# Kernel tuning notes

Hardware: AMD Instinct MI355X
Metric: run time of the kernel (lower is better)

## Reference

```python
import jax, jax.numpy as jnp
import numpy as np
from jax import lax

SIGMA = 2.0      # init arg
HIGH = 0.2       # init arg: high_threshold
LOW = 0.1        # skimage canny default low_threshold for float images
MAX_ITERS = 256  # cap for hysteresis propagation


def _conv2(img, kern):
    # img (N,1,H,W), kern (kh,kw); reflect-padded 'same' convolution
    kh, kw = kern.shape
    p = jnp.pad(img, ((0, 0), (0, 0), (kh // 2, kh // 2), (kw // 2, kw // 2)), mode='reflect')
    k = kern[None, None].astype(img.dtype)
    return lax.conv_general_dilated(p, k, (1, 1), 'VALID')


def _canny(x):
    # x (N,1,H,W) in [0,1] -> binary edge maps (N,H,W) float32
    r = int(4.0 * SIGMA + 0.5)
    g1 = np.exp(-0.5 * (np.arange(-r, r + 1) / SIGMA) ** 2)
    g1 = (g1 / g1.sum()).astype(np.float32)
    # separable gaussian blur
    sm = _conv2(_conv2(x, jnp.asarray(g1[:, None])), jnp.asarray(g1[None, :]))
    # sobel gradients
    sob = jnp.asarray([[-1., 0., 1.], [-2., 0., 2.], [-1., 0., 1.]], jnp.float32)
    gx = _conv2(sm, sob)[:, 0]
    gy = _conv2(sm, sob.T)[:, 0]          # (N,H,W)
    mag = jnp.hypot(gx, gy)
    ang = jnp.degrees(jnp.arctan2(gy, gx)) % 180.0
    N, H, W = mag.shape
    mp = jnp.pad(mag, ((0, 0), (1, 1), (1, 1)))
    sh = lambda dy, dx: mp[:, 1 + dy:1 + dy + H, 1 + dx:1 + dx + W]
    # quantize gradient direction into 4 bins for non-max suppression
    b0 = (ang < 22.5) | (ang >= 157.5)            # horizontal gradient -> E/W neighbors
    b1 = (ang >= 22.5) & (ang < 67.5)             # 45 deg
    b2 = (ang >= 67.5) & (ang < 112.5)            # vertical
    n1 = jnp.where(b0, sh(0, 1), jnp.where(b1, sh(-1, 1), jnp.where(b2, sh(-1, 0), sh(-1, -1))))
    n2 = jnp.where(b0, sh(0, -1), jnp.where(b1, sh(1, -1), jnp.where(b2, sh(1, 0), sh(1, 1))))
    keep = (mag >= n1) & (mag >= n2)
    strong = keep & (mag > HIGH)
    weak = keep & (mag > LOW)

    def dilate(s):
        f = lax.reduce_window(s.astype(jnp.float32), -jnp.inf, lax.max, (1, 3, 3), (1, 1, 1), 'SAME')
        return f > 0.0

    # hysteresis: propagate strong labels through weak pixels until fixpoint
    def cond(c):
        return c[1] & (c[2] < MAX_ITERS)

    def body(c):
        s, _, it = c
        ns = (dilate(s) & weak) | s
        return ns, jnp.any(ns != s), it + 1

    strong, _, _ = lax.while_loop(cond, body, (strong, jnp.array(True), jnp.array(0, jnp.int32)))
    return strong.astype(jnp.float32)


def setup_inputs() -> dict:
    key = jax.random.key(0)
    k1, k2, k3 = jax.random.split(key, 3)
    N, H, W = 16, 1024, 1024
    x = jax.random.uniform(k1, (N, 1, H, W), jnp.float32)
    y = jax.random.uniform(k2, (N, 1, H, W), jnp.float32)
    mask = jax.random.uniform(k3, (H, W), jnp.float32)
    return {"x": x, "y": y, "mask": mask}


def reference(x, y, mask):
    # original detaches x before canny -> edges carry no gradient
    edges = lax.stop_gradient(_canny(x))          # (N,H,W)
    # sum over batch of per-sample mean L1 (nn.L1Loss default reduction='mean')
    diff = jnp.abs(edges * mask - y[:, 0] * mask)
    return jnp.sum(jnp.mean(diff, axis=(1, 2)))
```

## Files before the change

### kernel.cpp

```cpp
#include <hip/hip_runtime.h>
#include <cmath>

#define IMG_W   1024
#define IMG_H   1024
#define NIMG    16
#define HW      (1024 * 1024)
#define NHW     (16 * 1024 * 1024)
#define WPR     16
#define WPI     (IMG_H * WPR)

struct GW { float w[9]; };

__device__ __forceinline__ int refl(int v) {
    return v < 0 ? -v : (v > 1023 ? 2046 - v : v);
}

__global__ void blur_v(const float* __restrict__ in, float* __restrict__ out, GW g) {
    int gid = blockIdx.x * 256 + threadIdx.x;
    int c4  = gid & 255;
    int rc  = (gid >> 8) & 127;
    const float* img = in  + (size_t)(gid >> 15) * HW;
    float*      outp = out + (size_t)(gid >> 15) * HW;
    int y0 = rc * 8;
    float4 acc[8];
#pragma unroll
    for (int j = 0; j < 8; ++j) acc[j] = make_float4(0.f, 0.f, 0.f, 0.f);
#pragma unroll
    for (int d = -8; d <= 15; ++d) {
        int rr = refl(y0 + d);
        float4 v = *(const float4*)(img + rr * IMG_W + c4 * 4);
#pragma unroll
        for (int j = 0; j < 8; ++j) {
            int k = d - j;
            if (k >= -8 && k <= 8) {
                float wt = g.w[k < 0 ? -k : k];
                acc[j].x += wt * v.x; acc[j].y += wt * v.y;
                acc[j].z += wt * v.z; acc[j].w += wt * v.w;
            }
        }
    }
#pragma unroll
    for (int j = 0; j < 8; ++j)
        *(float4*)(outp + (y0 + j) * IMG_W + c4 * 4) = acc[j];
}

__global__ void __launch_bounds__(256)
hgradnms(const float* __restrict__ vb, unsigned long long* __restrict__ strongw,
         unsigned long long* __restrict__ weakw, GW g) {
    __shared__ float smem[68 * 84 + 68 * 72];
    float* VB = smem;
    float* S  = smem + 68 * 84;
    float* M  = smem;
    unsigned char* Bn = (unsigned char*)(smem + 66 * 68);

    int tid = threadIdx.x;
    int b   = blockIdx.x;
    int img = b >> 8;
    int tr  = (b >> 4) & 15, tc = b & 15;
    int r0  = tr * 64, c0 = tc * 64;
    const float* vimg = vb + (size_t)img * HW;

    for (int i = tid; i < 68 * 84; i += 256) {
        int l = i / 84, m = i % 84;
        int gr = refl(r0 + l - 2);
        int gc = refl(c0 + m - 10);
        VB[i] = vimg[gr * IMG_W + gc];
    }
    __syncthreads();

    for (int i = tid; i < 68 * 17; i += 256) {
        int l = i / 17, grp = i % 17;
        const float4* p = (const float4*)(VB + l * 84 + 4 * grp);
        float w20[20];
        ((float4*)w20)[0] = p[0]; ((float4*)w20)[1] = p[1]; ((float4*)w20)[2] = p[2];
        ((float4*)w20)[3] = p[3]; ((float4*)w20)[4] = p[4];
        float o[4] = {0.f, 0.f, 0.f, 0.f};
#pragma unroll
        for (int t = 0; t < 17; ++t) {
            float wt = g.w[t < 8 ? 8 - t : t - 8];
#pragma unroll
            for (int j = 0; j < 4; ++j) o[j] += wt * w20[j + t];
        }
        *(float4*)(S + l * 72 + 4 * grp) = make_float4(o[0], o[1], o[2], o[3]);
    }
    __syncthreads();

    const float T1 = 0.41421356237309503f;
    const float T2 = 2.41421356237309510f;
    for (int i = tid; i < 66 * 17; i += 256) {
        int row = i / 17, grp = i % 17;
        float ra[8], rb[8], rcw[8];
        ((float4*)ra)[0]  = *(const float4*)(S + (row    ) * 72 + 4 * grp);
        ((float4*)ra)[1]  = *(const float4*)(S + (row    ) * 72 + 4 * grp + 4);
        ((float4*)rb)[0]  = *(const float4*)(S + (row + 1) * 72 + 4 * grp);
        ((float4*)rb)[1]  = *(const float4*)(S + (row + 1) * 72 + 4 * grp + 4);
        ((float4*)rcw)[0] = *(const float4*)(S + (row + 2) * 72 + 4 * grp);
        ((float4*)rcw)[1] = *(const float4*)(S + (row + 2) * 72 + 4 * grp + 4);
        int pr = r0 + row - 1;
        bool rin = (unsigned)pr <= 1023u;
#pragma unroll
        for (int j = 0; j < 4; ++j) {
            int colidx = 4 * grp + j;
            if (colidx > 65) continue;
            int pc = c0 + colidx - 1;
            bool in = rin && ((unsigned)pc <= 1023u);
            float a00 = ra[j], a01 = ra[j + 1], a02 = ra[j + 2];
            float a10 = rb[j],                  a12 = rb[j + 2];
            float a20 = rcw[j], a21 = rcw[j + 1], a22 = rcw[j + 2];
            float gx = (a02 - a00) + 2.f * (a12 - a10) + (a22 - a20);
            float gy = (a20 + 2.f * a21 + a22) - (a00 + 2.f * a01 + a02);
            float mv = in ? sqrtf(gx * gx + gy * gy) : 0.f;
            M[row * 68 + colidx] = mv;
            if (row >= 1 && row <= 64 && colidx >= 1 && colidx <= 64) {
                float ax = fabsf(gx), ay = fabsf(gy);
                int bn;
                if (ay < T1 * ax)      bn = 0;
                else if (ay > T2 * ax) bn = 2;
                else                   bn = ((gx > 0.f) == (gy > 0.f)) ? 1 : 3;
                Bn[(row - 1) * 64 + (colidx - 1)] = (unsigned char)bn;
            }
        }
    }
    __syncthreads();

    int lane = tid & 63, wv = tid >> 6;
    unsigned long long* sgw = strongw + (size_t)img * WPI;
    unsigned long long* wkw = weakw   + (size_t)img * WPI;
    for (int it = 0; it < 16; ++it) {
        int qr = wv * 16 + it;
        int qc = lane;
        float cm = M[(qr + 1) * 68 + qc + 1];
        int bn = Bn[qr * 64 + qc];
        int d1y = (bn == 0) ? 0 : -1;
        int d1x = (bn < 2) ? 1 : ((bn == 2) ? 0 : -1);
        float n1 = M[(qr + 1 + d1y) * 68 + (qc + 1 + d1x)];
        float n2 = M[(qr + 1 - d1y) * 68 + (qc + 1 - d1x)];
        bool keep   = (cm >= n1) && (cm >= n2);
        bool strong = keep && (cm > 0.2f);
        bool weak   = keep && (cm > 0.1f);
        unsigned long long sb = __ballot(strong);
        unsigned long long wb = __ballot(weak);
        if (lane == 0) {
            int widx = (r0 + qr) * WPR + tc;
            sgw[widx] = sb;
            wkw[widx] = wb;
        }
    }
}

__global__ void __launch_bounds__(1024, 1)
hyst(unsigned long long* __restrict__ strongw, const unsigned long long* __restrict__ weakw) {
    __shared__ unsigned long long S[WPI];
    __shared__ int chg;
    unsigned long long* sg = strongw + (size_t)blockIdx.x * WPI;
    const unsigned long long* wk = weakw + (size_t)blockIdx.x * WPI;
    int t = threadIdx.x;
    int c = t & 15;
    int rbase = (t >> 4) * 16;

    unsigned long long ww[16];
#pragma unroll
    for (int i = 0; i < 16; ++i) {
        S[(rbase + i) * WPR + c] = sg[(rbase + i) * WPR + c];
        ww[i] = wk[(rbase + i) * WPR + c];
    }
    __syncthreads();

    for (int pass = 0; pass < 4096; ++pass) {
        if (t == 0) chg = 0;
        __syncthreads();
        int any = 0;
        auto step = [&](int r, unsigned long long wwv) {
            unsigned long long w = S[r * WPR + c];
            if (!(wwv & ~w)) return;
            unsigned long long up = 0, dn = 0, upl = 0, upr = 0, dnl = 0, dnr = 0, ml = 0, mr = 0;
            if (r > 0)    { up = S[(r - 1) * WPR + c];
                            if (c > 0)  upl = S[(r - 1) * WPR + c - 1];
                            if (c < 15) upr = S[(r - 1) * WPR + c + 1]; }
            if (r < 1023) { dn = S[(r + 1) * WPR + c];
                            if (c > 0)  dnl = S[(r + 1) * WPR + c - 1];
                            if (c < 15) dnr = S[(r + 1) * WPR + c + 1]; }
            if (c > 0)  ml = S[r * WPR + c - 1];
            if (c < 15) mr = S[r * WPR + c + 1];
            unsigned long long H =
                  up | (up << 1) | (up >> 1) | (upl >> 63) | (upr << 63)
                | w  | (w  << 1) | (w  >> 1) | (ml  >> 63) | (mr  << 63)
                | dn | (dn << 1) | (dn >> 1) | (dnl >> 63) | (dnr << 63);
            unsigned long long nw = w | (H & wwv);
            for (;;) {
                unsigned long long nn = nw | (((nw << 1) | (nw >> 1)) & wwv);
                if (nn == nw) break;
                nw = nn;
            }
            if (nw != w) { S[r * WPR + c] = nw; any = 1; }
        };
        if (!(pass & 1)) {
#pragma unroll
            for (int i = 0; i < 16; ++i) step(rbase + i, ww[i]);
        } else {
#pragma unroll
            for (int i = 15; i >= 0; --i) step(rbase + i, ww[i]);
        }
        if (any) chg = 1;
        __syncthreads();
        int done = (chg == 0);
        __syncthreads();
        if (done) break;
    }
#pragma unroll
    for (int i = 0; i < 16; ++i) sg[(rbase + i) * WPR + c] = S[(rbase + i) * WPR + c];
}

__global__ void loss_part(const unsigned long long* __restrict__ strongw,
                          const float* __restrict__ y, const float* __restrict__ mask,
                          float* __restrict__ part) {
    int tid = threadIdx.x;
    float local = 0.f;
    const float4* y4 = (const float4*)y;
    const float4* m4 = (const float4*)mask;
    for (int i4 = blockIdx.x * 256 + tid; i4 < NHW / 4; i4 += 2048 * 256) {
        unsigned long long wword = strongw[i4 >> 4];
        int sh = (i4 & 15) * 4;
        unsigned bits = (unsigned)((wword >> sh) & 0xFull);
        float4 yv = y4[i4];
        float4 mv = m4[i4 & (HW / 4 - 1)];
        local += fabsf(((bits & 1u) ? mv.x : 0.f) - yv.x * mv.x);
        local += fabsf(((bits & 2u) ? mv.y : 0.f) - yv.y * mv.y);
        local += fabsf(((bits & 4u) ? mv.z : 0.f) - yv.z * mv.z);
        local += fabsf(((bits & 8u) ? mv.w : 0.f) - yv.w * mv.w);
    }
    for (int off = 32; off; off >>= 1) local += __shfl_down(local, off);
    __shared__ float wsum[4];
    if ((tid & 63) == 0) wsum[tid >> 6] = local;
    __syncthreads();
    if (tid == 0) part[blockIdx.x] = wsum[0] + wsum[1] + wsum[2] + wsum[3];
}

__global__ void loss_final(const float* __restrict__ part, float* __restrict__ out) {
    int tid = threadIdx.x;
    double s = 0.0;
    for (int i = tid; i < 2048; i += 256) s += (double)part[i];
    for (int off = 32; off; off >>= 1) s += __shfl_down(s, off);
    __shared__ double ws4[4];
    if ((tid & 63) == 0) ws4[tid >> 6] = s;
    __syncthreads();
    if (tid == 0) out[0] = (float)((ws4[0] + ws4[1] + ws4[2] + ws4[3]) * (1.0 / (double)HW));
}

extern "C" void kernel_launch(void* const* d_in, const int* in_sizes, int n_in,
                              void* d_out, int out_size, void* d_ws, size_t ws_size,
                              hipStream_t stream) {
    const float* x    = (const float*)d_in[0];
    const float* y    = (const float*)d_in[1];
    const float* mask = (const float*)d_in[2];
    float* out = (float*)d_out;

    char* ws = (char*)d_ws;
    float* vbuf = (float*)(ws);
    unsigned long long* strongw = (unsigned long long*)(ws + (size_t)64 * 1024 * 1024);
    unsigned long long* weakw   = (unsigned long long*)(ws + (size_t)66 * 1024 * 1024);
    float* part = (float*)(ws + (size_t)68 * 1024 * 1024);

    GW g;
    {
        double e[9], s;
        for (int k = 0; k < 9; ++k) e[k] = std::exp(-0.5 * (k / 2.0) * (k / 2.0));
        s = e[0];
        for (int k = 1; k < 9; ++k) s += 2.0 * e[k];
        for (int k = 0; k < 9; ++k) g.w[k] = (float)(e[k] / s);
    }

    blur_v    <<<2048, 256, 0, stream>>>(x, vbuf, g);
    hgradnms  <<<4096, 256, 0, stream>>>(vbuf, strongw, weakw, g);
    hyst      <<<NIMG, 1024, 0, stream>>>(strongw, weakw);
    loss_part <<<2048, 256, 0, stream>>>(strongw, y, mask, part);
    loss_final<<<1, 256, 0, stream>>>(part, out);
}
```

Baseline: 354.5 us.

## Shrink hgradnms shared memory to one aliased buffer and vectorize halo loads

The separate blur-input and blurred-row shared buffers are merged into a single 68x88 buffer that is reused in place. Each stage now holds its results in registers, syncs, then writes them back over the same buffer, and launch bounds request five blocks per CU. Interior tiles load the halo with aligned float4 global reads instead of scalar reflected loads, and direction bins are packed four per word with a padded layout. The cost is two extra barriers per stage and more register pressure under the tighter occupancy target.

```diff
diff --git a/kernel.cpp b/kernel.cpp
--- a/kernel.cpp
+++ b/kernel.cpp
@@ -44,14 +44,11 @@
         *(float4*)(outp + (y0 + j) * IMG_W + c4 * 4) = acc[j];
 }
 
-__global__ void __launch_bounds__(256)
+__global__ void __launch_bounds__(256, 5)
 hgradnms(const float* __restrict__ vb, unsigned long long* __restrict__ strongw,
          unsigned long long* __restrict__ weakw, GW g) {
-    __shared__ float smem[68 * 84 + 68 * 72];
-    float* VB = smem;
-    float* S  = smem + 68 * 84;
-    float* M  = smem;
-    unsigned char* Bn = (unsigned char*)(smem + 66 * 68);
+    __shared__ float L[68 * 88];
+    unsigned char* Bn = (unsigned char*)(L + 66 * 68);
 
     int tid = threadIdx.x;
     int b   = blockIdx.x;
@@ -60,65 +57,103 @@
     int r0  = tr * 64, c0 = tc * 64;
     const float* vimg = vb + (size_t)img * HW;
 
-    for (int i = tid; i < 68 * 84; i += 256) {
-        int l = i / 84, m = i % 84;
-        int gr = refl(r0 + l - 2);
-        int gc = refl(c0 + m - 10);
-        VB[i] = vimg[gr * IMG_W + gc];
-    }
-    __syncthreads();
-
-    for (int i = tid; i < 68 * 17; i += 256) {
-        int l = i / 17, grp = i % 17;
-        const float4* p = (const float4*)(VB + l * 84 + 4 * grp);
-        float w20[20];
-        ((float4*)w20)[0] = p[0]; ((float4*)w20)[1] = p[1]; ((float4*)w20)[2] = p[2];
-        ((float4*)w20)[3] = p[3]; ((float4*)w20)[4] = p[4];
-        float o[4] = {0.f, 0.f, 0.f, 0.f};
-#pragma unroll
-        for (int t = 0; t < 17; ++t) {
-            float wt = g.w[t < 8 ? 8 - t : t - 8];
-#pragma unroll
-            for (int j = 0; j < 4; ++j) o[j] += wt * w20[j + t];
-        }
-        *(float4*)(S + l * 72 + 4 * grp) = make_float4(o[0], o[1], o[2], o[3]);
+    if (tc > 0 && tc < 15) {
+        const float* basep = vimg + (c0 - 12);
+        for (int i = tid; i < 68 * 22; i += 256) {
+            int l = i / 22, q = i % 22;
+            int gr = refl(r0 + l - 2);
+            *(float4*)(L + l * 88 + 4 * q) = *(const float4*)(basep + gr * IMG_W + 4 * q);
+        }
+    } else {
+        for (int i = tid; i < 68 * 88; i += 256) {
+            int l = i / 88, m = i % 88;
+            int gr = refl(r0 + l - 2);
+            int gc = refl(c0 - 12 + m);
+            L[i] = vimg[gr * IMG_W + gc];
+        }
+    }
+    __syncthreads();
+
+    float4 oreg[5];
+#pragma unroll
+    for (int it = 0; it < 5; ++it) {
+        int i = tid + it * 256;
+        if (i < 68 * 17) {
+            int l = i / 17, gq = i % 17;
+            float w24[24];
+#pragma unroll
+            for (int q = 0; q < 6; ++q)
+                ((float4*)w24)[q] = *(const float4*)(L + l * 88 + 4 * gq + 4 * q);
+            float o0 = 0.f, o1 = 0.f, o2 = 0.f, o3 = 0.f;
+#pragma unroll
+            for (int t = 0; t < 17; ++t) {
+                float wt = g.w[t < 8 ? 8 - t : t - 8];
+                o0 += wt * w24[2 + t]; o1 += wt * w24[3 + t];
+                o2 += wt * w24[4 + t]; o3 += wt * w24[5 + t];
+            }
+            oreg[it] = make_float4(o0, o1, o2, o3);
+        }
+    }
+    __syncthreads();
+#pragma unroll
+    for (int it = 0; it < 5; ++it) {
+        int i = tid + it * 256;
+        if (i < 68 * 17) {
+            int l = i / 17, gq = i % 17;
+            *(float4*)(L + l * 88 + 4 * gq) = oreg[it];
+        }
     }
     __syncthreads();
 
     const float T1 = 0.41421356237309503f;
     const float T2 = 2.41421356237309510f;
-    for (int i = tid; i < 66 * 17; i += 256) {
-        int row = i / 17, grp = i % 17;
-        float ra[8], rb[8], rcw[8];
-        ((float4*)ra)[0]  = *(const float4*)(S + (row    ) * 72 + 4 * grp);
-        ((float4*)ra)[1]  = *(const float4*)(S + (row    ) * 72 + 4 * grp + 4);
-        ((float4*)rb)[0]  = *(const float4*)(S + (row + 1) * 72 + 4 * grp);
-        ((float4*)rb)[1]  = *(const float4*)(S + (row + 1) * 72 + 4 * grp + 4);
-        ((float4*)rcw)[0] = *(const float4*)(S + (row + 2) * 72 + 4 * grp);
-        ((float4*)rcw)[1] = *(const float4*)(S + (row + 2) * 72 + 4 * grp + 4);
-        int pr = r0 + row - 1;
-        bool rin = (unsigned)pr <= 1023u;
-#pragma unroll
-        for (int j = 0; j < 4; ++j) {
-            int colidx = 4 * grp + j;
-            if (colidx > 65) continue;
-            int pc = c0 + colidx - 1;
-            bool in = rin && ((unsigned)pc <= 1023u);
-            float a00 = ra[j], a01 = ra[j + 1], a02 = ra[j + 2];
-            float a10 = rb[j],                  a12 = rb[j + 2];
-            float a20 = rcw[j], a21 = rcw[j + 1], a22 = rcw[j + 2];
-            float gx = (a02 - a00) + 2.f * (a12 - a10) + (a22 - a20);
-            float gy = (a20 + 2.f * a21 + a22) - (a00 + 2.f * a01 + a02);
-            float mv = in ? sqrtf(gx * gx + gy * gy) : 0.f;
-            M[row * 68 + colidx] = mv;
-            if (row >= 1 && row <= 64 && colidx >= 1 && colidx <= 64) {
+    float4 mreg[5];
+    unsigned int breg[5];
+#pragma unroll
+    for (int it = 0; it < 5; ++it) {
+        int i = tid + it * 256;
+        if (i < 66 * 17) {
+            int row = i / 17, gq = i % 17;
+            float ra[8], rb[8], rc8[8];
+            ((float4*)ra)[0]  = *(const float4*)(L + (row    ) * 88 + 4 * gq);
+            ((float4*)ra)[1]  = *(const float4*)(L + (row    ) * 88 + 4 * gq + 4);
+            ((float4*)rb)[0]  = *(const float4*)(L + (row + 1) * 88 + 4 * gq);
+            ((float4*)rb)[1]  = *(const float4*)(L + (row + 1) * 88 + 4 * gq + 4);
+            ((float4*)rc8)[0] = *(const float4*)(L + (row + 2) * 88 + 4 * gq);
+            ((float4*)rc8)[1] = *(const float4*)(L + (row + 2) * 88 + 4 * gq + 4);
+            int pr = r0 + row - 1;
+            bool rin = (unsigned)pr <= 1023u;
+            float mv[4]; unsigned int bpk = 0;
+#pragma unroll
+            for (int j = 0; j < 4; ++j) {
+                int colidx = 4 * gq + j;
+                float a00 = ra[j], a01 = ra[j + 1], a02 = ra[j + 2];
+                float a10 = rb[j],                   a12 = rb[j + 2];
+                float a20 = rc8[j], a21 = rc8[j + 1], a22 = rc8[j + 2];
+                float gx = (a02 - a00) + 2.f * (a12 - a10) + (a22 - a20);
+                float gy = (a20 + 2.f * a21 + a22) - (a00 + 2.f * a01 + a02);
+                int pc = c0 + colidx - 1;
+                bool in = rin && ((unsigned)pc <= 1023u) && (colidx <= 65);
+                mv[j] = in ? sqrtf(gx * gx + gy * gy) : 0.f;
                 float ax = fabsf(gx), ay = fabsf(gy);
                 int bn;
                 if (ay < T1 * ax)      bn = 0;
                 else if (ay > T2 * ax) bn = 2;
                 else                   bn = ((gx > 0.f) == (gy > 0.f)) ? 1 : 3;
-                Bn[(row - 1) * 64 + (colidx - 1)] = (unsigned char)bn;
+                bpk |= (unsigned)bn << (8 * j);
             }
+            mreg[it] = make_float4(mv[0], mv[1], mv[2], mv[3]);
+            breg[it] = bpk;
+        }
+    }
+    __syncthreads();
+#pragma unroll
+    for (int it = 0; it < 5; ++it) {
+        int i = tid + it * 256;
+        if (i < 66 * 17) {
+            int row = i / 17, gq = i % 17;
+            *(float4*)(L + row * 68 + 4 * gq) = mreg[it];
+            *(unsigned int*)(Bn + row * 68 + 4 * gq) = breg[it];
         }
     }
     __syncthreads();
@@ -129,12 +164,12 @@
     for (int it = 0; it < 16; ++it) {
         int qr = wv * 16 + it;
         int qc = lane;
-        float cm = M[(qr + 1) * 68 + qc + 1];
-        int bn = Bn[qr * 64 + qc];
+        float cm = L[(qr + 1) * 68 + qc + 1];
+        int bn = Bn[(qr + 1) * 68 + qc + 1];
         int d1y = (bn == 0) ? 0 : -1;
         int d1x = (bn < 2) ? 1 : ((bn == 2) ? 0 : -1);
-        float n1 = M[(qr + 1 + d1y) * 68 + (qc + 1 + d1x)];
-        float n2 = M[(qr + 1 - d1y) * 68 + (qc + 1 - d1x)];
+        float n1 = L[(qr + 1 + d1y) * 68 + (qc + 1 + d1x)];
+        float n2 = L[(qr + 1 - d1y) * 68 + (qc + 1 - d1x)];
         bool keep   = (cm >= n1) && (cm >= n2);
         bool strong = keep && (cm > 0.2f);
         bool weak   = keep && (cm > 0.1f);
```

Result: faster. 339.4 us (-4.2%).
